# Kernel tuning notes

Measured on AMD Instinct MI355X. Metric: run time of the kernel, lower is better.

Reference implementation:

```python
import jax, jax.numpy as jnp
import numpy as np

K_SIZE = 5  # local window size (odd, SAME padding, stride 1)


def _local_attn(x_main, x_ref, W_main, W_ref, k_size=K_SIZE):
    # 1x1 convs == per-pixel channel matmuls
    cm = jnp.einsum('bhwc,cd->bhwd', x_main, W_main)  # query  [B,H,W,C']
    cr = jnp.einsum('bhwc,cd->bhwd', x_ref, W_ref)    # keys   [B,H,W,C']
    pad = (k_size - 1) // 2
    B, H, W, C = cr.shape
    crp = jnp.pad(cr, ((0, 0), (pad, pad), (pad, pad), (0, 0)))
    # score for each of the k*k offsets: dot(query, shifted key) per pixel.
    # Avoids materializing the [B,H,W,k*k,C] patch tensor.
    scores = [
        jnp.einsum('bhwc,bhwc->bhw', cm, crp[:, i:i + H, j:j + W, :])
        for i in range(k_size) for j in range(k_size)
    ]
    # the layer concatenates the query itself as the last "key" (self score)
    scores.append(jnp.einsum('bhwc,bhwc->bhw', cm, cm))
    attn = jnp.stack(scores, axis=-1)  # [B,H,W,k*k+1]
    return jax.nn.softmax(attn, axis=-1)


def setup_inputs() -> dict:
    key = jax.random.key(0)
    k1, k2, k3, k4 = jax.random.split(key, 4)
    B, H, W, C = 4, 128, 128, 64
    Ci = 64  # intermediate_dim
    return {
        'x_main': jax.random.normal(k1, (B, H, W, C), jnp.float32),
        'x_ref': jax.random.normal(k2, (B, H, W, C), jnp.float32),
        'W_main': jax.random.normal(k3, (C, Ci), jnp.float32) * (2.0 / C) ** 0.5,
        'W_ref': jax.random.normal(k4, (C, Ci), jnp.float32) * (2.0 / C) ** 0.5,
    }


def reference(x_main, x_ref, W_main, W_ref):
    return _local_attn(x_main, x_ref, W_main, W_ref)
```

## Files before the change

### kernel.cpp

```cpp
#include <hip/hip_runtime.h>
#include <math.h>

#define HDIM 128
#define WDIM 128
#define CDIM 64
#define BDIM 4
#define NPIX (BDIM * HDIM * WDIM)

typedef short bf16x8 __attribute__((ext_vector_type(8)));
typedef float f32x4  __attribute__((ext_vector_type(4)));

__device__ __forceinline__ void split_bf16(float f, short& hi, short& lo) {
    unsigned u = __float_as_uint(f);
    hi = (short)(u >> 16);
    float hf = __uint_as_float(u & 0xffff0000u);
    float l  = f - hf;
    lo = (short)(__float_as_uint(l) >> 16);
}

__global__ __launch_bounds__(256, 1)
void conv1x1_mfma_kernel(const float* __restrict__ xm,
                         const float* __restrict__ xr,
                         const float* __restrict__ Wm,
                         const float* __restrict__ Wr,
                         float* __restrict__ outm,
                         float* __restrict__ outr) {
    const float* x; const float* Wg; float* out;
    if (blockIdx.y == 0) { x = xm; Wg = Wm; out = outm; }
    else                 { x = xr; Wg = Wr; out = outr; }

    __shared__ float Wsh[CDIM * CDIM];
    const int t = threadIdx.x;
    {
        const float4* Wg4 = (const float4*)Wg;
        float4* Ws4 = (float4*)Wsh;
        #pragma unroll
        for (int i = 0; i < 4; ++i) Ws4[t + 256 * i] = Wg4[t + 256 * i];
    }
    __syncthreads();

    const int lane = t & 63;
    const int wv   = t >> 6;
    const int m    = lane & 15;
    const int quad = lane >> 4;

    bf16x8 Bhi[2][4], Blo[2][4];
    #pragma unroll
    for (int ks = 0; ks < 2; ++ks) {
        #pragma unroll
        for (int nt = 0; nt < 4; ++nt) {
            #pragma unroll
            for (int j = 0; j < 8; ++j) {
                float f = Wsh[(ks * 32 + quad * 8 + j) * CDIM + nt * 16 + m];
                short hi, lo; split_bf16(f, hi, lo);
                Bhi[ks][nt][j] = hi;
                Blo[ks][nt][j] = lo;
            }
        }
    }

    const int tbase = (blockIdx.x * 4 + wv) * 4;

    float4 pa[4][4];
    #pragma unroll
    for (int it = 0; it < 4; ++it) {
        const float* ap = x + ((size_t)((tbase + it) * 16 + m)) * CDIM + quad * 8;
        pa[it][0] = *(const float4*)(ap);
        pa[it][1] = *(const float4*)(ap + 4);
        pa[it][2] = *(const float4*)(ap + 32);
        pa[it][3] = *(const float4*)(ap + 36);
    }

    #pragma unroll
    for (int it = 0; it < 4; ++it) {
        bf16x8 Ahi[2], Alo[2];
        #pragma unroll
        for (int ks = 0; ks < 2; ++ks) {
            float fv[8];
            float4 p = pa[it][2 * ks], q = pa[it][2 * ks + 1];
            fv[0] = p.x; fv[1] = p.y; fv[2] = p.z; fv[3] = p.w;
            fv[4] = q.x; fv[5] = q.y; fv[6] = q.z; fv[7] = q.w;
            #pragma unroll
            for (int j = 0; j < 8; ++j) {
                short hi, lo; split_bf16(fv[j], hi, lo);
                Ahi[ks][j] = hi;
                Alo[ks][j] = lo;
            }
        }

        f32x4 acc[4];
        #pragma unroll
        for (int nt = 0; nt < 4; ++nt) {
            acc[nt][0] = 0.f; acc[nt][1] = 0.f;
            acc[nt][2] = 0.f; acc[nt][3] = 0.f;
        }
        #pragma unroll
        for (int ks = 0; ks < 2; ++ks) {
            #pragma unroll
            for (int nt = 0; nt < 4; ++nt) {
                acc[nt] = __builtin_amdgcn_mfma_f32_16x16x32_bf16(
                              Ahi[ks], Bhi[ks][nt], acc[nt], 0, 0, 0);
                acc[nt] = __builtin_amdgcn_mfma_f32_16x16x32_bf16(
                              Ahi[ks], Blo[ks][nt], acc[nt], 0, 0, 0);
                acc[nt] = __builtin_amdgcn_mfma_f32_16x16x32_bf16(
                              Alo[ks], Bhi[ks][nt], acc[nt], 0, 0, 0);
            }
        }

        float* op = out + ((size_t)((tbase + it) * 16 + quad * 4)) * CDIM + m;
        #pragma unroll
        for (int nt = 0; nt < 4; ++nt) {
            #pragma unroll
            for (int r = 0; r < 4; ++r)
                op[(size_t)r * CDIM + nt * 16] = acc[nt][r];
        }
    }
}

#define TILE_W 16
#define TILE_H 8
#define HALO_W 20
#define HALO_H 12
#define NHALO (HALO_W * HALO_H)
#define PSTRIDE 68

__global__ __launch_bounds__(256, 1)
void attn_tiled_kernel(const float* __restrict__ cm,
                       const float* __restrict__ cr,
                       float* __restrict__ out) {
    __shared__ float crs[NHALO * PSTRIDE];

    const int t   = threadIdx.x;
    const int tx0 = blockIdx.x * TILE_W;
    const int ty0 = blockIdx.y * TILE_H;
    const int b   = blockIdx.z;

    #pragma unroll
    for (int it = 0; it < 15; ++it) {
        int L   = t + 256 * it;
        int pix = L >> 4;
        int q   = L & 15;
        int hy  = pix / HALO_W;
        int hx  = pix - hy * HALO_W;
        int gy  = ty0 + hy - 2, gx = tx0 + hx - 2;
        float4 v = make_float4(0.f, 0.f, 0.f, 0.f);
        if (gy >= 0 && gy < HDIM && gx >= 0 && gx < WDIM) {
            size_t gp = ((size_t)b * HDIM + gy) * WDIM + gx;
            v = *(const float4*)&cr[gp * CDIM + 4 * q];
        }
        *(float4*)&crs[pix * PSTRIDE + 4 * q] = v;
    }
    __syncthreads();

    const int pl = t >> 1;
    const int cg = t & 1;
    const int lx = pl & (TILE_W - 1);
    const int ly = pl >> 4;
    const size_t gpx = ((size_t)b * HDIM + ty0 + ly) * WDIM + tx0 + lx;

    float4 qv[8];
    {
        const float4* cmp = (const float4*)&cm[gpx * CDIM + cg * 32];
        #pragma unroll
        for (int mq = 0; mq < 8; ++mq) qv[mq] = cmp[mq];
    }

    float s[26];
    #pragma unroll
    for (int k = 0; k < 25; ++k) {
        const int i = k / 5, j = k % 5;
        const int p = (ly + i) * HALO_W + (lx + j);
        const float4* kp = (const float4*)&crs[p * PSTRIDE + cg * 32];
        float acc = 0.f;
        #pragma unroll
        for (int mq = 0; mq < 8; ++mq) {
            float4 v = kp[mq];
            acc = fmaf(qv[mq].x, v.x, acc);
            acc = fmaf(qv[mq].y, v.y, acc);
            acc = fmaf(qv[mq].z, v.z, acc);
            acc = fmaf(qv[mq].w, v.w, acc);
        }
        s[k] = acc;
    }
    {
        float acc = 0.f;
        #pragma unroll
        for (int mq = 0; mq < 8; ++mq) {
            float4 v = qv[mq];
            acc = fmaf(v.x, v.x, acc);
            acc = fmaf(v.y, v.y, acc);
            acc = fmaf(v.z, v.z, acc);
            acc = fmaf(v.w, v.w, acc);
        }
        s[25] = acc;
    }

    #pragma unroll
    for (int k = 0; k < 26; ++k) s[k] += __shfl_xor(s[k], 1);

    float mx = s[0];
    #pragma unroll
    for (int k = 1; k < 26; ++k) mx = fmaxf(mx, s[k]);
    float sum = 0.f;
    #pragma unroll
    for (int k = 0; k < 26; ++k) { s[k] = __expf(s[k] - mx); sum += s[k]; }
    const float inv = 1.f / sum;

    float* op = &out[gpx * 26 + cg * 13];
    if (cg == 0) {
        #pragma unroll
        for (int k = 0; k < 13; ++k) op[k] = s[k] * inv;
    } else {
        #pragma unroll
        for (int k = 0; k < 13; ++k) op[k] = s[13 + k] * inv;
    }
}

extern "C" void kernel_launch(void* const* d_in, const int* in_sizes, int n_in,
                              void* d_out, int out_size, void* d_ws, size_t ws_size,
                              hipStream_t stream) {
    const float* xm = (const float*)d_in[0];
    const float* xr = (const float*)d_in[1];
    const float* Wm = (const float*)d_in[2];
    const float* Wr = (const float*)d_in[3];
    float* outp = (float*)d_out;

    float* cm = (float*)d_ws;
    float* cr = cm + (size_t)NPIX * CDIM;

    dim3 g1(256, 2);
    conv1x1_mfma_kernel<<<g1, 256, 0, stream>>>(xm, xr, Wm, Wr, cm, cr);

    dim3 g2(WDIM / TILE_W, HDIM / TILE_H, BDIM);
    attn_tiled_kernel<<<g2, 256, 0, stream>>>(cm, cr, outp);
}
```

Measured before the change: 99.07 us.

## Fuse 1x1 conv projections into tiled local-attention kernel, recomputing key halo

Merges the two kernels into one. Each block computes the query projection for its 16x8 tile and the key projection for its 20x12 halo with split-bf16 MFMA, writing both into LDS instead of round-tripping through a global workspace. This removes the global write and re-read of the projected tensors and one kernel launch. In exchange, key projections in the halo are recomputed redundantly (about 1.9x the key work), and block-level LDS reuse requires extra barriers.

```diff
diff --git a/kernel.cpp b/kernel.cpp
--- a/kernel.cpp
+++ b/kernel.cpp
@@ -5,7 +5,14 @@
 #define WDIM 128
 #define CDIM 64
 #define BDIM 4
-#define NPIX (BDIM * HDIM * WDIM)
+
+#define TILE_W 16
+#define TILE_H 8
+#define HALO_W 20
+#define HALO_H 12
+#define NHALO (HALO_W * HALO_H)
+#define PSTRIDE 68
+#define WSTRIDE 65
 
 typedef short bf16x8 __attribute__((ext_vector_type(8)));
 typedef float f32x4  __attribute__((ext_vector_type(4)));
@@ -19,151 +26,165 @@
 }
 
 __global__ __launch_bounds__(256, 1)
-void conv1x1_mfma_kernel(const float* __restrict__ xm,
-                         const float* __restrict__ xr,
-                         const float* __restrict__ Wm,
-                         const float* __restrict__ Wr,
-                         float* __restrict__ outm,
-                         float* __restrict__ outr) {
-    const float* x; const float* Wg; float* out;
-    if (blockIdx.y == 0) { x = xm; Wg = Wm; out = outm; }
-    else                 { x = xr; Wg = Wr; out = outr; }
-
-    __shared__ float Wsh[CDIM * CDIM];
-    const int t = threadIdx.x;
-    {
-        const float4* Wg4 = (const float4*)Wg;
-        float4* Ws4 = (float4*)Wsh;
-        #pragma unroll
-        for (int i = 0; i < 4; ++i) Ws4[t + 256 * i] = Wg4[t + 256 * i];
-    }
-    __syncthreads();
-
+void fused_mfma_local_attn(const float* __restrict__ xm,
+                           const float* __restrict__ xr,
+                           const float* __restrict__ Wm,
+                           const float* __restrict__ Wr,
+                           float* __restrict__ out) {
+    __shared__ float lds[16320];
+    float* Wsh = lds;
+    float* cms = lds + 4352;
+    float* crs = lds;
+
+    const int t    = threadIdx.x;
     const int lane = t & 63;
     const int wv   = t >> 6;
     const int m    = lane & 15;
     const int quad = lane >> 4;
+    const int tx0  = blockIdx.x * TILE_W;
+    const int ty0  = blockIdx.y * TILE_H;
+    const int b    = blockIdx.z;
+
+    #pragma unroll
+    for (int i = 0; i < 16; ++i) {
+        int L = t + 256 * i;
+        Wsh[(L >> 6) * WSTRIDE + (L & 63)] = Wm[L];
+    }
+    __syncthreads();
 
     bf16x8 Bhi[2][4], Blo[2][4];
     #pragma unroll
-    for (int ks = 0; ks < 2; ++ks) {
-        #pragma unroll
-        for (int nt = 0; nt < 4; ++nt) {
+    for (int ks = 0; ks < 2; ++ks)
+        #pragma unroll
+        for (int nt = 0; nt < 4; ++nt)
             #pragma unroll
             for (int j = 0; j < 8; ++j) {
-                float f = Wsh[(ks * 32 + quad * 8 + j) * CDIM + nt * 16 + m];
+                float f = Wsh[(ks * 32 + quad * 8 + j) * WSTRIDE + nt * 16 + m];
                 short hi, lo; split_bf16(f, hi, lo);
-                Bhi[ks][nt][j] = hi;
-                Blo[ks][nt][j] = lo;
-            }
-        }
-    }
-
-    const int tbase = (blockIdx.x * 4 + wv) * 4;
-
-    float4 pa[4][4];
-    #pragma unroll
-    for (int it = 0; it < 4; ++it) {
-        const float* ap = x + ((size_t)((tbase + it) * 16 + m)) * CDIM + quad * 8;
-        pa[it][0] = *(const float4*)(ap);
-        pa[it][1] = *(const float4*)(ap + 4);
-        pa[it][2] = *(const float4*)(ap + 32);
-        pa[it][3] = *(const float4*)(ap + 36);
-    }
-
-    #pragma unroll
-    for (int it = 0; it < 4; ++it) {
+                Bhi[ks][nt][j] = hi; Blo[ks][nt][j] = lo;
+            }
+
+    #pragma unroll
+    for (int s = 0; s < 2; ++s) {
+        const int tile = 2 * wv + s;
+        const float* ap = xm + (((size_t)b * HDIM + ty0 + tile) * WDIM
+                                + tx0 + m) * CDIM + quad * 8;
+        float4 p0 = *(const float4*)(ap);
+        float4 p1 = *(const float4*)(ap + 4);
+        float4 p2 = *(const float4*)(ap + 32);
+        float4 p3 = *(const float4*)(ap + 36);
+
         bf16x8 Ahi[2], Alo[2];
-        #pragma unroll
-        for (int ks = 0; ks < 2; ++ks) {
-            float fv[8];
-            float4 p = pa[it][2 * ks], q = pa[it][2 * ks + 1];
-            fv[0] = p.x; fv[1] = p.y; fv[2] = p.z; fv[3] = p.w;
-            fv[4] = q.x; fv[5] = q.y; fv[6] = q.z; fv[7] = q.w;
+        {
+            float fv[16] = {p0.x,p0.y,p0.z,p0.w, p1.x,p1.y,p1.z,p1.w,
+                            p2.x,p2.y,p2.z,p2.w, p3.x,p3.y,p3.z,p3.w};
+            #pragma unroll
+            for (int ks = 0; ks < 2; ++ks)
+                #pragma unroll
+                for (int j = 0; j < 8; ++j) {
+                    short hi, lo; split_bf16(fv[8 * ks + j], hi, lo);
+                    Ahi[ks][j] = hi; Alo[ks][j] = lo;
+                }
+        }
+        f32x4 acc[4];
+        #pragma unroll
+        for (int nt = 0; nt < 4; ++nt)
+            { acc[nt][0]=0.f; acc[nt][1]=0.f; acc[nt][2]=0.f; acc[nt][3]=0.f; }
+        #pragma unroll
+        for (int ks = 0; ks < 2; ++ks)
+            #pragma unroll
+            for (int nt = 0; nt < 4; ++nt) {
+                acc[nt] = __builtin_amdgcn_mfma_f32_16x16x32_bf16(Ahi[ks], Bhi[ks][nt], acc[nt], 0,0,0);
+                acc[nt] = __builtin_amdgcn_mfma_f32_16x16x32_bf16(Ahi[ks], Blo[ks][nt], acc[nt], 0,0,0);
+                acc[nt] = __builtin_amdgcn_mfma_f32_16x16x32_bf16(Alo[ks], Bhi[ks][nt], acc[nt], 0,0,0);
+            }
+        #pragma unroll
+        for (int nt = 0; nt < 4; ++nt)
+            #pragma unroll
+            for (int r = 0; r < 4; ++r)
+                cms[(tile * 16 + quad * 4 + r) * PSTRIDE + nt * 16 + m] = acc[nt][r];
+    }
+    __syncthreads();
+
+    #pragma unroll
+    for (int i = 0; i < 16; ++i) {
+        int L = t + 256 * i;
+        Wsh[(L >> 6) * WSTRIDE + (L & 63)] = Wr[L];
+    }
+    __syncthreads();
+
+    #pragma unroll
+    for (int ks = 0; ks < 2; ++ks)
+        #pragma unroll
+        for (int nt = 0; nt < 4; ++nt)
             #pragma unroll
             for (int j = 0; j < 8; ++j) {
-                short hi, lo; split_bf16(fv[j], hi, lo);
-                Ahi[ks][j] = hi;
-                Alo[ks][j] = lo;
-            }
-        }
-
-        f32x4 acc[4];
-        #pragma unroll
-        for (int nt = 0; nt < 4; ++nt) {
-            acc[nt][0] = 0.f; acc[nt][1] = 0.f;
-            acc[nt][2] = 0.f; acc[nt][3] = 0.f;
-        }
-        #pragma unroll
-        for (int ks = 0; ks < 2; ++ks) {
-            #pragma unroll
-            for (int nt = 0; nt < 4; ++nt) {
-                acc[nt] = __builtin_amdgcn_mfma_f32_16x16x32_bf16(
-                              Ahi[ks], Bhi[ks][nt], acc[nt], 0, 0, 0);
-                acc[nt] = __builtin_amdgcn_mfma_f32_16x16x32_bf16(
-                              Ahi[ks], Blo[ks][nt], acc[nt], 0, 0, 0);
-                acc[nt] = __builtin_amdgcn_mfma_f32_16x16x32_bf16(
-                              Alo[ks], Bhi[ks][nt], acc[nt], 0, 0, 0);
-            }
-        }
-
-        float* op = out + ((size_t)((tbase + it) * 16 + quad * 4)) * CDIM + m;
-        #pragma unroll
-        for (int nt = 0; nt < 4; ++nt) {
-            #pragma unroll
-            for (int r = 0; r < 4; ++r)
-                op[(size_t)r * CDIM + nt * 16] = acc[nt][r];
-        }
-    }
-}
-
-#define TILE_W 16
-#define TILE_H 8
-#define HALO_W 20
-#define HALO_H 12
-#define NHALO (HALO_W * HALO_H)
-#define PSTRIDE 68
-
-__global__ __launch_bounds__(256, 1)
-void attn_tiled_kernel(const float* __restrict__ cm,
-                       const float* __restrict__ cr,
-                       float* __restrict__ out) {
-    __shared__ float crs[NHALO * PSTRIDE];
-
-    const int t   = threadIdx.x;
-    const int tx0 = blockIdx.x * TILE_W;
-    const int ty0 = blockIdx.y * TILE_H;
-    const int b   = blockIdx.z;
-
-    #pragma unroll
-    for (int it = 0; it < 15; ++it) {
-        int L   = t + 256 * it;
-        int pix = L >> 4;
-        int q   = L & 15;
-        int hy  = pix / HALO_W;
-        int hx  = pix - hy * HALO_W;
-        int gy  = ty0 + hy - 2, gx = tx0 + hx - 2;
-        float4 v = make_float4(0.f, 0.f, 0.f, 0.f);
-        if (gy >= 0 && gy < HDIM && gx >= 0 && gx < WDIM) {
-            size_t gp = ((size_t)b * HDIM + gy) * WDIM + gx;
-            v = *(const float4*)&cr[gp * CDIM + 4 * q];
-        }
-        *(float4*)&crs[pix * PSTRIDE + 4 * q] = v;
-    }
-    __syncthreads();
+                float f = Wsh[(ks * 32 + quad * 8 + j) * WSTRIDE + nt * 16 + m];
+                short hi, lo; split_bf16(f, hi, lo);
+                Bhi[ks][nt][j] = hi; Blo[ks][nt][j] = lo;
+            }
 
     const int pl = t >> 1;
     const int cg = t & 1;
+    float4 qv[8];
+    #pragma unroll
+    for (int mq = 0; mq < 8; ++mq)
+        qv[mq] = *(const float4*)&cms[pl * PSTRIDE + cg * 32 + 4 * mq];
+    __syncthreads();
+
+    #pragma unroll
+    for (int s = 0; s < 4; ++s) {
+        const int tj = wv + 4 * s;
+        if (tj < 15) {
+            const int hp = tj * 16 + m;
+            const int hy = hp / HALO_W;
+            const int hx = hp - hy * HALO_W;
+            const int gy = ty0 + hy - 2, gx = tx0 + hx - 2;
+            float4 p0 = make_float4(0,0,0,0), p1 = p0, p2 = p0, p3 = p0;
+            if (gy >= 0 && gy < HDIM && gx >= 0 && gx < WDIM) {
+                const float* ap = xr + (((size_t)b * HDIM + gy) * WDIM + gx) * CDIM
+                                  + quad * 8;
+                p0 = *(const float4*)(ap);
+                p1 = *(const float4*)(ap + 4);
+                p2 = *(const float4*)(ap + 32);
+                p3 = *(const float4*)(ap + 36);
+            }
+            bf16x8 Ahi[2], Alo[2];
+            {
+                float fv[16] = {p0.x,p0.y,p0.z,p0.w, p1.x,p1.y,p1.z,p1.w,
+                                p2.x,p2.y,p2.z,p2.w, p3.x,p3.y,p3.z,p3.w};
+                #pragma unroll
+                for (int ks = 0; ks < 2; ++ks)
+                    #pragma unroll
+                    for (int j = 0; j < 8; ++j) {
+                        short hi, lo; split_bf16(fv[8 * ks + j], hi, lo);
+                        Ahi[ks][j] = hi; Alo[ks][j] = lo;
+                    }
+            }
+            f32x4 acc[4];
+            #pragma unroll
+            for (int nt = 0; nt < 4; ++nt)
+                { acc[nt][0]=0.f; acc[nt][1]=0.f; acc[nt][2]=0.f; acc[nt][3]=0.f; }
+            #pragma unroll
+            for (int ks = 0; ks < 2; ++ks)
+                #pragma unroll
+                for (int nt = 0; nt < 4; ++nt) {
+                    acc[nt] = __builtin_amdgcn_mfma_f32_16x16x32_bf16(Ahi[ks], Bhi[ks][nt], acc[nt], 0,0,0);
+                    acc[nt] = __builtin_amdgcn_mfma_f32_16x16x32_bf16(Ahi[ks], Blo[ks][nt], acc[nt], 0,0,0);
+                    acc[nt] = __builtin_amdgcn_mfma_f32_16x16x32_bf16(Alo[ks], Bhi[ks][nt], acc[nt], 0,0,0);
+                }
+            #pragma unroll
+            for (int nt = 0; nt < 4; ++nt)
+                #pragma unroll
+                for (int r = 0; r < 4; ++r)
+                    crs[(tj * 16 + quad * 4 + r) * PSTRIDE + nt * 16 + m] = acc[nt][r];
+        }
+    }
+    __syncthreads();
+
     const int lx = pl & (TILE_W - 1);
     const int ly = pl >> 4;
     const size_t gpx = ((size_t)b * HDIM + ty0 + ly) * WDIM + tx0 + lx;
-
-    float4 qv[8];
-    {
-        const float4* cmp = (const float4*)&cm[gpx * CDIM + cg * 32];
-        #pragma unroll
-        for (int mq = 0; mq < 8; ++mq) qv[mq] = cmp[mq];
-    }
 
     float s[26];
     #pragma unroll
@@ -225,12 +246,6 @@
     const float* Wr = (const float*)d_in[3];
     float* outp = (float*)d_out;
 
-    float* cm = (float*)d_ws;
-    float* cr = cm + (size_t)NPIX * CDIM;
-
-    dim3 g1(256, 2);
-    conv1x1_mfma_kernel<<<g1, 256, 0, stream>>>(xm, xr, Wm, Wr, cm, cr);
-
-    dim3 g2(WDIM / TILE_W, HDIM / TILE_H, BDIM);
-    attn_tiled_kernel<<<g2, 256, 0, stream>>>(cm, cr, outp);
+    dim3 g(WDIM / TILE_W, HDIM / TILE_H, BDIM);
+    fused_mfma_local_attn<<<g, 256, 0, stream>>>(xm, xr, Wm, Wr, outp);
 }
```

After: 89.87 us (median of 2 runs). 1.1x faster.
